# Optimization experiments

Measured on AMD Instinct MI355X. Metric: run time of the kernel, lower is better.

## Reference

```python
import jax, jax.numpy as jnp
import numpy as np

B, T, C = 1, 4096, 1024   # batch, seq, n_embd
E, K = 64, 8              # num_experts, router top-k
G, TG = 8, 4              # n_group, topk_group
H, HS = 512, 2048         # expert hidden, shared-expert hidden
STD = 0.02


def setup_inputs() -> dict:
    key = jax.random.key(0)
    ks = jax.random.split(key, 9)
    return {
        "x": jax.random.normal(ks[0], (B, T, C), jnp.float32),
        "router_w": jax.random.normal(ks[1], (E, C), jnp.float32) * (C ** -0.5),
        "e_bias": jnp.zeros((E,), jnp.float32),  # e_score_correction_bias buffer
        "gate_w": jax.random.normal(ks[2], (E, C, H), jnp.float32) * STD,
        "up_w": jax.random.normal(ks[3], (E, C, H), jnp.float32) * STD,
        "down_w": jax.random.normal(ks[4], (E, H, C), jnp.float32) * STD,
        "sh_gate_w": jax.random.normal(ks[5], (C, HS), jnp.float32) * STD,
        "sh_up_w": jax.random.normal(ks[6], (C, HS), jnp.float32) * STD,
        "sh_down_w": jax.random.normal(ks[7], (HS, C), jnp.float32) * STD,
    }


def _route(xf, router_w, e_bias):
    # grouped sigmoid top-k routing with score-correction bias (group_limited_greedy)
    S = xf.shape[0]
    scores = jax.nn.sigmoid(xf @ router_w.T)          # [S,E], raw sigmoid scores
    sb = scores + e_bias                               # biased scores (selection only)
    epg = E // G
    # per-group score = sum of top (K // topk_group) biased scores in that group
    grp = jax.lax.top_k(sb.reshape(S, G, epg), K // TG)[0].sum(-1)   # [S,G]
    gidx = jax.lax.top_k(grp, TG)[1]                                 # [S,TG]
    gmask = jnp.zeros((S, G), bool).at[jnp.arange(S)[:, None], gidx].set(True)
    emask = jnp.repeat(gmask, epg, axis=1)                           # [S,E]
    masked = jnp.where(emask, sb, -jnp.inf)
    topk_idx = jax.lax.top_k(masked, K)[1]                           # [S,K]
    w = jnp.take_along_axis(scores, topk_idx, axis=1)                # raw scores gathered
    w = w / (w.sum(-1, keepdims=True) + 1e-20)                       # norm_topk_prob
    return topk_idx, w


def reference(x, router_w, e_bias, gate_w, up_w, down_w, sh_gate_w, sh_up_w, sh_down_w):
    Bq, Tq, Cq = x.shape
    xf = x.reshape(Bq * Tq, Cq)
    # always-on shared expert (SwiGLU)
    shared = (jax.nn.silu(xf @ sh_gate_w) * (xf @ sh_up_w)) @ sh_down_w
    topk_idx, w = _route(xf, router_w, e_bias)
    fe = topk_idx.reshape(-1)                          # [S*K] expert id per routed row
    order = jnp.argsort(fe, stable=True)               # sort rows by expert (grouped)
    tok = order // K                                   # source token of each sorted row
    sorted_x = xf[tok]                                 # [S*K, C]
    group_sizes = jnp.bincount(fe, length=E).astype(jnp.int32)
    # grouped GEMMs (== torch._grouped_mm / bmm-over-buckets in the original)
    g = jax.lax.ragged_dot(sorted_x, gate_w, group_sizes)
    u = jax.lax.ragged_dot(sorted_x, up_w, group_sizes)
    h = jax.nn.silu(g) * u
    o = jax.lax.ragged_dot(h, down_w, group_sizes)     # [S*K, C]
    o = o * w.reshape(-1)[order][:, None]              # weight by routing prob
    routed = jnp.zeros_like(xf).at[tok].add(o)         # combine back per token
    return (shared + routed).reshape(Bq, Tq, Cq)
```

## Files before the change

### kernel.cpp

```cpp
#include <hip/hip_runtime.h>
#include <hip/hip_bf16.h>
#include <stdint.h>


#define S_TOK 4096
#define C_DIM 1024
#define E_NUM 64
#define H_DIM 512
#define HS_DIM 2048
#define ROWS_TOTAL (S_TOK * 8)

typedef __attribute__((ext_vector_type(8))) short short8;
typedef __attribute__((ext_vector_type(4))) float f32x4;

static __device__ __forceinline__ unsigned short f2bf(float f) {
    union { float f; uint32_t u; } v; v.f = f;
    uint32_t u = v.u;
    u += 0x7fffu + ((u >> 16) & 1u);
    return (unsigned short)(u >> 16);
}

static __device__ __forceinline__ void gl2lds16(const void* g, void* l) {
    __builtin_amdgcn_global_load_lds(
        (const __attribute__((address_space(1))) uint32_t*)g,
        (__attribute__((address_space(3))) uint32_t*)l, 16, 0, 0);
}

__global__ __launch_bounds__(256)
void router_scores_k(const float* __restrict__ x, const float* __restrict__ rw,
                     float* __restrict__ scores) {
    int t0 = blockIdx.x * 32;
    __shared__ float xs[32][36];
    __shared__ float wsm[64][36];
    int t = threadIdx.x;
    int tx = t & 15, ty = t >> 4;
    float acc[2][4] = {};
    for (int k0 = 0; k0 < C_DIM; k0 += 32) {
        {
            int r = t >> 3, c = t & 7;
            *(float4*)&xs[r][c * 4] = *(const float4*)(x + (size_t)(t0 + r) * C_DIM + k0 + c * 4);
        }
        #pragma unroll
        for (int i = 0; i < 2; i++) {
            int idx = t + 256 * i;
            int r = idx >> 3, c = idx & 7;
            *(float4*)&wsm[r][c * 4] = *(const float4*)(rw + (size_t)r * C_DIM + k0 + c * 4);
        }
        __syncthreads();
        #pragma unroll
        for (int kk = 0; kk < 32; kk += 4) {
            float4 a0 = *(const float4*)&xs[ty * 2 + 0][kk];
            float4 a1 = *(const float4*)&xs[ty * 2 + 1][kk];
            #pragma unroll
            for (int j = 0; j < 4; j++) {
                float4 b = *(const float4*)&wsm[tx * 4 + j][kk];
                acc[0][j] += a0.x * b.x + a0.y * b.y + a0.z * b.z + a0.w * b.w;
                acc[1][j] += a1.x * b.x + a1.y * b.y + a1.z * b.z + a1.w * b.w;
            }
        }
        __syncthreads();
    }
    #pragma unroll
    for (int i = 0; i < 2; i++)
        #pragma unroll
        for (int j = 0; j < 4; j++)
            scores[(size_t)(t0 + ty * 2 + i) * E_NUM + tx * 4 + j] =
                1.f / (1.f + __expf(-acc[i][j]));
}

__global__ __launch_bounds__(256)
void topk_k(const float* __restrict__ scores, const float* __restrict__ ebias,
            int* __restrict__ topk_idx, float* __restrict__ topk_w,
            int* __restrict__ counts) {
    int t = blockIdx.x * 4 + (threadIdx.x >> 6);
    int e = threadIdx.x & 63;
    float sc = scores[(size_t)t * E_NUM + e];
    float sb = sc + ebias[e];
    float m1 = sb, m2 = -1e30f;
    #pragma unroll
    for (int off = 1; off <= 4; off <<= 1) {
        float o1 = __shfl_xor(m1, off);
        float o2 = __shfl_xor(m2, off);
        float hi = fmaxf(m1, o1), lo = fminf(m1, o1);
        m2 = fmaxf(lo, fmaxf(m2, o2));
        m1 = hi;
    }
    float grp = m1 + m2;
    float grpv[8];
    #pragma unroll
    for (int g = 0; g < 8; g++) grpv[g] = __shfl(grp, g * 8);
    unsigned gsel = 0;
    #pragma unroll
    for (int k = 0; k < 4; k++) {
        float best = -1e30f; int bi = 0;
        #pragma unroll
        for (int g = 0; g < 8; g++)
            if (!((gsel >> g) & 1) && grpv[g] > best) { best = grpv[g]; bi = g; }
        gsel |= 1u << bi;
    }
    float val = ((gsel >> (e >> 3)) & 1) ? sb : -1e30f;
    int idx[8]; float sv[8]; float wsum = 0.f;
    #pragma unroll
    for (int k = 0; k < 8; k++) {
        uint32_t u = __float_as_uint(val);
        uint32_t mu = (u & 0x80000000u) ? ~u : (u | 0x80000000u);
        unsigned long long key = ((unsigned long long)mu << 6) | (unsigned long long)(63 - e);
        #pragma unroll
        for (int off = 32; off; off >>= 1) {
            unsigned long long ok = __shfl_xor(key, off);
            if (ok > key) key = ok;
        }
        int win = 63 - (int)(key & 63ull);
        idx[k] = win;
        sv[k] = __shfl(sc, win);
        wsum += sv[k];
        if (e == win) val = -1e30f;
    }
    float inv = 1.f / (wsum + 1e-20f);
    if (e < 8) {
        topk_idx[t * 8 + e] = idx[e];
        topk_w[t * 8 + e] = sv[e] * inv;
        atomicAdd(&counts[idx[e]], 1);
    }
}

__global__ void zero_counts_k(int* counts) { counts[threadIdx.x] = 0; }

__global__ void scan_k(const int* __restrict__ counts, int* __restrict__ base,
                       int* __restrict__ cursor) {
    if (threadIdx.x == 0) {
        int s = 0;
        for (int e = 0; e < E_NUM; e++) { base[e] = s; cursor[e] = s; s += counts[e]; }
    }
}

__global__ void scatter_k(const int* __restrict__ topk_idx, const float* __restrict__ topk_w,
                          int* __restrict__ cursor, int* __restrict__ row_token,
                          float* __restrict__ row_wgt) {
    int i = blockIdx.x * blockDim.x + threadIdx.x;
    int e = topk_idx[i];
    int pos = atomicAdd(&cursor[e], 1);
    row_token[pos] = i >> 3;
    row_wgt[pos] = topk_w[i];
}

__global__ void cvt_bf16_k(const float* __restrict__ in, unsigned short* __restrict__ out, int n8) {
    int i = blockIdx.x * blockDim.x + threadIdx.x;
    if (i >= n8) return;
    float4 v0 = ((const float4*)in)[2 * i];
    float4 v1 = ((const float4*)in)[2 * i + 1];
    unsigned short t[8] = { f2bf(v0.x), f2bf(v0.y), f2bf(v0.z), f2bf(v0.w),
                            f2bf(v1.x), f2bf(v1.y), f2bf(v1.z), f2bf(v1.w) };
    ((uint4*)out)[i] = *(uint4*)t;
}

#define TP 69
__global__ __launch_bounds__(256)
void transpose_k(const float* __restrict__ in, unsigned short* __restrict__ out, int R, int C) {
    size_t bofs = (size_t)blockIdx.z * R * C;
    in += bofs; out += bofs;
    int r0 = blockIdx.y * 64, c0 = blockIdx.x * 64;
    __shared__ float T[64 * TP];
    int t = threadIdx.x;
    int cg = t & 15, rg = t >> 4;
    #pragma unroll
    for (int ii = 0; ii < 4; ii++) {
        float4 v = *(const float4*)(in + (size_t)(r0 + rg * 4 + ii) * C + c0 + cg * 4);
        T[(cg * 4 + 0) * TP + rg * 4 + ii] = v.x;
        T[(cg * 4 + 1) * TP + rg * 4 + ii] = v.y;
        T[(cg * 4 + 2) * TP + rg * 4 + ii] = v.z;
        T[(cg * 4 + 3) * TP + rg * 4 + ii] = v.w;
    }
    __syncthreads();
    int n = t >> 2, ks = (t & 3) * 16;
    unsigned short h[16];
    #pragma unroll
    for (int u = 0; u < 16; u++) h[u] = f2bf(T[n * TP + ks + u]);
    unsigned short* op = out + (size_t)(c0 + n) * R + r0 + ks;
    *(uint4*)op = *(uint4*)&h[0];
    *(uint4*)(op + 8) = *(uint4*)&h[8];
}

template<bool FUSED, bool GATHER, bool GROUPED, int EPI>
__global__ __launch_bounds__(256, 2)
void gemm2_k(const short* __restrict__ A, const short* __restrict__ B1t,
             const short* __restrict__ B2t, void* __restrict__ Cout,
             int M, int N, int K,
             const int* __restrict__ counts, const int* __restrict__ base,
             const int* __restrict__ row_token, const float* __restrict__ row_wgt) {
    int e = GROUPED ? blockIdx.z : 0;
    int Mrows = GROUPED ? counts[e] : M;
    int n0 = blockIdx.x * 128;
    int rowbase = GROUPED ? base[e] : 0;
    const short* B1 = B1t + (GROUPED ? (size_t)e * N * K : 0) + (size_t)n0 * K;
    const short* B2 = FUSED ? (B2t + (GROUPED ? (size_t)e * N * K : 0) + (size_t)n0 * K) : nullptr;

    __shared__ short As[2 * 4096];
    __shared__ short Bs1[2 * 4096];
    __shared__ short Bs2[FUSED ? 2 * 4096 : 16];

    int tid = threadIdx.x;
    int lane = tid & 63, w = tid >> 6;
    int wr = w >> 1, wc = w & 1;
    int quad = lane >> 4, l16 = lane & 15;
    int sr = lane >> 2, sc = lane & 3;

    for (int m0 = blockIdx.y * 128; m0 < Mrows; m0 += gridDim.y * 128) {
        const short* aptr[2];
        const short* b1ptr[2];
        const short* b2ptr[2];
        #pragma unroll
        for (int i = 0; i < 2; i++) {
            int row = w * 32 + i * 16 + sr;
            int mrow = m0 + row;
            int cl = mrow < Mrows ? mrow : (Mrows - 1);
            size_t arow;
            if (GATHER)       arow = (size_t)row_token[rowbase + cl];
            else if (GROUPED) arow = (size_t)(rowbase + cl);
            else              arow = (size_t)mrow;
            aptr[i] = A + arow * K + sc * 8;
            b1ptr[i] = B1 + (size_t)row * K + sc * 8;
            if (FUSED) b2ptr[i] = B2 + (size_t)row * K + sc * 8;
        }

        f32x4 acc1[4][4] = {};
        f32x4 acc2[4][4] = {};

        const int nk = K >> 5;
        #pragma unroll
        for (int i = 0; i < 2; i++) {
            int lb = (w * 32 + i * 16) * 32;
            gl2lds16(aptr[i], &As[lb]);   aptr[i] += 32;
            gl2lds16(b1ptr[i], &Bs1[lb]); b1ptr[i] += 32;
            if (FUSED) { gl2lds16(b2ptr[i], &Bs2[lb]); b2ptr[i] += 32; }
        }
        __syncthreads();

        for (int t = 0; t < nk; t++) {
            int bofs = (t & 1) * 4096;
            int nofs = 4096 - bofs;
            if (t + 1 < nk) {
                #pragma unroll
                for (int i = 0; i < 2; i++) {
                    int lb = nofs + (w * 32 + i * 16) * 32;
                    gl2lds16(aptr[i], &As[lb]);   aptr[i] += 32;
                    gl2lds16(b1ptr[i], &Bs1[lb]); b1ptr[i] += 32;
                    if (FUSED) { gl2lds16(b2ptr[i], &Bs2[lb]); b2ptr[i] += 32; }
                }
            }
            short8 a[4], b1[4], b2[4];
            #pragma unroll
            for (int i = 0; i < 4; i++)
                a[i] = *(const short8*)&As[bofs + (wr * 64 + i * 16 + l16) * 32 + quad * 8];
            #pragma unroll
            for (int j = 0; j < 4; j++) {
                b1[j] = *(const short8*)&Bs1[bofs + (wc * 64 + j * 16 + l16) * 32 + quad * 8];
                if (FUSED)
                    b2[j] = *(const short8*)&Bs2[bofs + (wc * 64 + j * 16 + l16) * 32 + quad * 8];
            }
            #pragma unroll
            for (int i = 0; i < 4; i++)
                #pragma unroll
                for (int j = 0; j < 4; j++) {
                    acc1[i][j] = __builtin_amdgcn_mfma_f32_16x16x32_bf16(a[i], b1[j], acc1[i][j], 0, 0, 0);
                    if (FUSED)
                        acc2[i][j] = __builtin_amdgcn_mfma_f32_16x16x32_bf16(a[i], b2[j], acc2[i][j], 0, 0, 0);
                }
            __syncthreads();
        }

        #pragma unroll
        for (int i = 0; i < 4; i++) {
            #pragma unroll
            for (int rr = 0; rr < 4; rr++) {
                int row = m0 + wr * 64 + i * 16 + quad * 4 + rr;
                if (row >= Mrows) continue;
                size_t orow = GROUPED ? (size_t)(rowbase + row) : (size_t)row;
                int tok = 0; float scl = 0.f;
                if (EPI == 2) { tok = row_token[rowbase + row]; scl = row_wgt[rowbase + row]; }
                #pragma unroll
                for (int j = 0; j < 4; j++) {
                    int n = n0 + wc * 64 + j * 16 + l16;
                    float v = acc1[i][j][rr];
                    if (EPI == 0) {
                        float u = acc2[i][j][rr];
                        float h = v / (1.f + __expf(-v)) * u;
                        ((unsigned short*)Cout)[orow * N + n] = f2bf(h);
                    } else if (EPI == 1) {
                        ((float*)Cout)[orow * N + n] = v;
                    } else {
                        atomicAdd(&((float*)Cout)[(size_t)tok * N + n], v * scl);
                    }
                }
            }
        }
    }
}

extern "C" void kernel_launch(void* const* d_in, const int* in_sizes, int n_in,
                              void* d_out, int out_size, void* d_ws, size_t ws_size,
                              hipStream_t stream) {
    const float* x        = (const float*)d_in[0];
    const float* router_w = (const float*)d_in[1];
    const float* e_bias   = (const float*)d_in[2];
    const float* gate_w   = (const float*)d_in[3];
    const float* up_w     = (const float*)d_in[4];
    const float* down_w   = (const float*)d_in[5];
    const float* sh_gate  = (const float*)d_in[6];
    const float* sh_up    = (const float*)d_in[7];
    const float* sh_down  = (const float*)d_in[8];
    float* out = (float*)d_out;
    char* ws = (char*)d_ws;

    int*   counts    = (int*)(ws);
    int*   base      = (int*)(ws + 256);
    int*   cursor    = (int*)(ws + 512);
    int*   topk_idx  = (int*)(ws + 1024);
    float* topk_w    = (float*)(ws + 1024 + 131072);
    int*   row_token = (int*)(ws + 1024 + 2 * 131072);
    float* row_wgt   = (float*)(ws + 1024 + 3 * 131072);
    float* scoresbuf = (float*)(ws + 1024 + 4 * 131072);
    const size_t MB = 1u << 20;
    unsigned short* xb        = (unsigned short*)(ws + 2 * MB);
    unsigned short* Hs        = (unsigned short*)(ws + 10 * MB);
    unsigned short* Hr        = (unsigned short*)(ws + 26 * MB);
    unsigned short* sh_gate_t = (unsigned short*)(ws + 58 * MB);
    unsigned short* sh_up_t   = (unsigned short*)(ws + 62 * MB);
    unsigned short* sh_down_t = (unsigned short*)(ws + 66 * MB);
    unsigned short* gate_t    = (unsigned short*)(ws + 70 * MB);
    unsigned short* up_t      = (unsigned short*)(ws + 134 * MB);
    unsigned short* down_t    = (unsigned short*)(ws + 198 * MB);

    zero_counts_k<<<1, 64, 0, stream>>>(counts);
    router_scores_k<<<S_TOK / 32, 256, 0, stream>>>(x, router_w, scoresbuf);
    topk_k<<<S_TOK / 4, 256, 0, stream>>>(scoresbuf, e_bias, topk_idx, topk_w, counts);
    scan_k<<<1, 64, 0, stream>>>(counts, base, cursor);
    scatter_k<<<ROWS_TOTAL / 256, 256, 0, stream>>>(topk_idx, topk_w, cursor, row_token, row_wgt);

    cvt_bf16_k<<<S_TOK * C_DIM / 8 / 256, 256, 0, stream>>>(x, xb, S_TOK * C_DIM / 8);
    transpose_k<<<dim3(HS_DIM / 64, C_DIM / 64, 1), 256, 0, stream>>>(sh_gate, sh_gate_t, C_DIM, HS_DIM);
    transpose_k<<<dim3(HS_DIM / 64, C_DIM / 64, 1), 256, 0, stream>>>(sh_up,   sh_up_t,   C_DIM, HS_DIM);
    transpose_k<<<dim3(C_DIM / 64, HS_DIM / 64, 1), 256, 0, stream>>>(sh_down, sh_down_t, HS_DIM, C_DIM);
    transpose_k<<<dim3(H_DIM / 64, C_DIM / 64, E_NUM), 256, 0, stream>>>(gate_w, gate_t, C_DIM, H_DIM);
    transpose_k<<<dim3(H_DIM / 64, C_DIM / 64, E_NUM), 256, 0, stream>>>(up_w,   up_t,   C_DIM, H_DIM);
    transpose_k<<<dim3(C_DIM / 64, H_DIM / 64, E_NUM), 256, 0, stream>>>(down_w, down_t, H_DIM, C_DIM);

    gemm2_k<true, false, false, 0><<<dim3(HS_DIM / 128, S_TOK / 128, 1), 256, 0, stream>>>(
        (const short*)xb, (const short*)sh_gate_t, (const short*)sh_up_t, Hs,
        S_TOK, HS_DIM, C_DIM, nullptr, nullptr, nullptr, nullptr);
    gemm2_k<false, false, false, 1><<<dim3(C_DIM / 128, S_TOK / 128, 1), 256, 0, stream>>>(
        (const short*)Hs, (const short*)sh_down_t, nullptr, out,
        S_TOK, C_DIM, HS_DIM, nullptr, nullptr, nullptr, nullptr);

    gemm2_k<true, true, true, 0><<<dim3(H_DIM / 128, 4, E_NUM), 256, 0, stream>>>(
        (const short*)xb, (const short*)gate_t, (const short*)up_t, Hr,
        0, H_DIM, C_DIM, counts, base, row_token, row_wgt);
    gemm2_k<false, false, true, 2><<<dim3(C_DIM / 128, 4, E_NUM), 256, 0, stream>>>(
        (const short*)Hr, (const short*)down_t, nullptr, out,
        0, C_DIM, H_DIM, counts, base, row_token, row_wgt);
}
```

Before: 1.018 ms.

## Triple-buffer GEMM LDS pipeline and replace atomic scatter-add with gather combine

The GEMM k-loop moves from double to triple buffering of the LDS tiles. Explicit vmcnt waits and a single barrier per iteration let global-to-LDS loads run two stages ahead, where before the loop synchronised twice per iteration. The routed down-projection now writes weighted rows to a dense fp32 buffer instead of doing atomicAdd into the output. A new combine kernel gathers each token's eight rows using a position map recorded during scatter. This removes atomic contention but adds a large extra write and read of that buffer. The expert-count scan also becomes a wavefront shuffle scan.

```diff
diff --git a/kernel.cpp b/kernel.cpp
--- a/kernel.cpp
+++ b/kernel.cpp
@@ -128,20 +128,45 @@
 
 __global__ void scan_k(const int* __restrict__ counts, int* __restrict__ base,
                        int* __restrict__ cursor) {
-    if (threadIdx.x == 0) {
-        int s = 0;
-        for (int e = 0; e < E_NUM; e++) { base[e] = s; cursor[e] = s; s += counts[e]; }
-    }
+    int e = threadIdx.x;
+    int c = counts[e];
+    int s = c;
+    #pragma unroll
+    for (int off = 1; off < 64; off <<= 1) {
+        int o = __shfl_up(s, off);
+        if (e >= off) s += o;
+    }
+    int ex = s - c;
+    base[e] = ex;
+    cursor[e] = ex;
 }
 
 __global__ void scatter_k(const int* __restrict__ topk_idx, const float* __restrict__ topk_w,
                           int* __restrict__ cursor, int* __restrict__ row_token,
-                          float* __restrict__ row_wgt) {
+                          float* __restrict__ row_wgt, int* __restrict__ pos_of) {
     int i = blockIdx.x * blockDim.x + threadIdx.x;
     int e = topk_idx[i];
     int pos = atomicAdd(&cursor[e], 1);
     row_token[pos] = i >> 3;
     row_wgt[pos] = topk_w[i];
+    pos_of[i] = pos;
+}
+
+__global__ __launch_bounds__(256)
+void combine_k(const float* __restrict__ O, const int* __restrict__ pos_of,
+               float* __restrict__ out) {
+    int t = blockIdx.x;
+    int c = threadIdx.x;
+    float4 s = ((const float4*)(out + (size_t)t * C_DIM))[c];
+    int p[8];
+    #pragma unroll
+    for (int k = 0; k < 8; k++) p[k] = pos_of[t * 8 + k];
+    #pragma unroll
+    for (int k = 0; k < 8; k++) {
+        float4 v = ((const float4*)(O + (size_t)p[k] * C_DIM))[c];
+        s.x += v.x; s.y += v.y; s.z += v.z; s.w += v.w;
+    }
+    ((float4*)(out + (size_t)t * C_DIM))[c] = s;
 }
 
 __global__ void cvt_bf16_k(const float* __restrict__ in, unsigned short* __restrict__ out, int n8) {
@@ -195,9 +220,9 @@
     const short* B1 = B1t + (GROUPED ? (size_t)e * N * K : 0) + (size_t)n0 * K;
     const short* B2 = FUSED ? (B2t + (GROUPED ? (size_t)e * N * K : 0) + (size_t)n0 * K) : nullptr;
 
-    __shared__ short As[2 * 4096];
-    __shared__ short Bs1[2 * 4096];
-    __shared__ short Bs2[FUSED ? 2 * 4096 : 16];
+    __shared__ short As[3 * 4096];
+    __shared__ short Bs1[3 * 4096];
+    __shared__ short Bs2[FUSED ? 3 * 4096 : 16];
 
     int tid = threadIdx.x;
     int lane = tid & 63, w = tid >> 6;
@@ -227,27 +252,32 @@
         f32x4 acc2[4][4] = {};
 
         const int nk = K >> 5;
-        #pragma unroll
-        for (int i = 0; i < 2; i++) {
-            int lb = (w * 32 + i * 16) * 32;
-            gl2lds16(aptr[i], &As[lb]);   aptr[i] += 32;
-            gl2lds16(b1ptr[i], &Bs1[lb]); b1ptr[i] += 32;
-            if (FUSED) { gl2lds16(b2ptr[i], &Bs2[lb]); b2ptr[i] += 32; }
-        }
-        __syncthreads();
-
+        auto stage = [&](int slot) {
+            #pragma unroll
+            for (int i = 0; i < 2; i++) {
+                int lb = slot * 4096 + (w * 32 + i * 16) * 32;
+                gl2lds16(aptr[i], &As[lb]);   aptr[i] += 32;
+                gl2lds16(b1ptr[i], &Bs1[lb]); b1ptr[i] += 32;
+                if (FUSED) { gl2lds16(b2ptr[i], &Bs2[lb]); b2ptr[i] += 32; }
+            }
+        };
+        stage(0);
+        if (nk > 1) stage(1);
+
+        int slot = 0, nslot = 2;
         for (int t = 0; t < nk; t++) {
-            int bofs = (t & 1) * 4096;
-            int nofs = 4096 - bofs;
             if (t + 1 < nk) {
-                #pragma unroll
-                for (int i = 0; i < 2; i++) {
-                    int lb = nofs + (w * 32 + i * 16) * 32;
-                    gl2lds16(aptr[i], &As[lb]);   aptr[i] += 32;
-                    gl2lds16(b1ptr[i], &Bs1[lb]); b1ptr[i] += 32;
-                    if (FUSED) { gl2lds16(b2ptr[i], &Bs2[lb]); b2ptr[i] += 32; }
-                }
-            }
+                if constexpr (FUSED) asm volatile("s_waitcnt vmcnt(6)" ::: "memory");
+                else                 asm volatile("s_waitcnt vmcnt(4)" ::: "memory");
+            } else {
+                asm volatile("s_waitcnt vmcnt(0)" ::: "memory");
+            }
+            __builtin_amdgcn_s_barrier();
+            __builtin_amdgcn_sched_barrier(0);
+
+            if (t + 2 < nk) stage(nslot);
+
+            int bofs = slot * 4096;
             short8 a[4], b1[4], b2[4];
             #pragma unroll
             for (int i = 0; i < 4; i++)
@@ -266,7 +296,8 @@
                     if (FUSED)
                         acc2[i][j] = __builtin_amdgcn_mfma_f32_16x16x32_bf16(a[i], b2[j], acc2[i][j], 0, 0, 0);
                 }
-            __syncthreads();
+            slot = (slot == 2) ? 0 : slot + 1;
+            nslot = (nslot == 2) ? 0 : nslot + 1;
         }
 
         #pragma unroll
@@ -276,8 +307,8 @@
                 int row = m0 + wr * 64 + i * 16 + quad * 4 + rr;
                 if (row >= Mrows) continue;
                 size_t orow = GROUPED ? (size_t)(rowbase + row) : (size_t)row;
-                int tok = 0; float scl = 0.f;
-                if (EPI == 2) { tok = row_token[rowbase + row]; scl = row_wgt[rowbase + row]; }
+                float scl = 0.f;
+                if (EPI == 2) scl = row_wgt[rowbase + row];
                 #pragma unroll
                 for (int j = 0; j < 4; j++) {
                     int n = n0 + wc * 64 + j * 16 + l16;
@@ -289,11 +320,12 @@
                     } else if (EPI == 1) {
                         ((float*)Cout)[orow * N + n] = v;
                     } else {
-                        atomicAdd(&((float*)Cout)[(size_t)tok * N + n], v * scl);
+                        ((float*)Cout)[orow * N + n] = v * scl;
                     }
                 }
             }
         }
+        __syncthreads();
     }
 }
 
@@ -320,6 +352,7 @@
     int*   row_token = (int*)(ws + 1024 + 2 * 131072);
     float* row_wgt   = (float*)(ws + 1024 + 3 * 131072);
     float* scoresbuf = (float*)(ws + 1024 + 4 * 131072);
+    int*   pos_of    = (int*)(ws + 1664 * 1024);
     const size_t MB = 1u << 20;
     unsigned short* xb        = (unsigned short*)(ws + 2 * MB);
     unsigned short* Hs        = (unsigned short*)(ws + 10 * MB);
@@ -330,12 +363,13 @@
     unsigned short* gate_t    = (unsigned short*)(ws + 70 * MB);
     unsigned short* up_t      = (unsigned short*)(ws + 134 * MB);
     unsigned short* down_t    = (unsigned short*)(ws + 198 * MB);
+    float* O = (float*)(ws + 70 * MB);
 
     zero_counts_k<<<1, 64, 0, stream>>>(counts);
     router_scores_k<<<S_TOK / 32, 256, 0, stream>>>(x, router_w, scoresbuf);
     topk_k<<<S_TOK / 4, 256, 0, stream>>>(scoresbuf, e_bias, topk_idx, topk_w, counts);
     scan_k<<<1, 64, 0, stream>>>(counts, base, cursor);
-    scatter_k<<<ROWS_TOTAL / 256, 256, 0, stream>>>(topk_idx, topk_w, cursor, row_token, row_wgt);
+    scatter_k<<<ROWS_TOTAL / 256, 256, 0, stream>>>(topk_idx, topk_w, cursor, row_token, row_wgt, pos_of);
 
     cvt_bf16_k<<<S_TOK * C_DIM / 8 / 256, 256, 0, stream>>>(x, xb, S_TOK * C_DIM / 8);
     transpose_k<<<dim3(HS_DIM / 64, C_DIM / 64, 1), 256, 0, stream>>>(sh_gate, sh_gate_t, C_DIM, HS_DIM);
@@ -356,6 +390,8 @@
         (const short*)xb, (const short*)gate_t, (const short*)up_t, Hr,
         0, H_DIM, C_DIM, counts, base, row_token, row_wgt);
     gemm2_k<false, false, true, 2><<<dim3(C_DIM / 128, 4, E_NUM), 256, 0, stream>>>(
-        (const short*)Hr, (const short*)down_t, nullptr, out,
+        (const short*)Hr, (const short*)down_t, nullptr, O,
         0, C_DIM, H_DIM, counts, base, row_token, row_wgt);
-}
+
+    combine_k<<<S_TOK, 256, 0, stream>>>(O, pos_of, out);
+}
```

New measurement: 994.6 us. 1.02x faster.
